# Kernel tuning notes

Measured on AMD Instinct MI355X. Metric: run time of the kernel, lower is better.

## Reference

```python
import jax, jax.numpy as jnp
import numpy as np

B, T, C, H = 4, 2048, 1024, 16
D = C // H


def setup_inputs() -> dict:
    key = jax.random.key(0)
    ks = jax.random.split(key, 5)
    s = 0.02
    return {
        "x": jax.random.normal(ks[0], (B, T, C), dtype=jnp.float32),
        "W_attn": jax.random.normal(ks[1], (C, 3 * C), dtype=jnp.float32) * s,
        "b_attn": jax.random.normal(ks[2], (3 * C,), dtype=jnp.float32) * s,
        "W_proj": jax.random.normal(ks[3], (C, C), dtype=jnp.float32) * s,
        "b_proj": jax.random.normal(ks[4], (C,), dtype=jnp.float32) * s,
    }


def reference(x, W_attn, b_attn, W_proj, b_proj):
    # QKV projection: [B,T,3C]
    qkv = x @ W_attn + b_attn
    q, k, v = jnp.split(qkv, 3, axis=-1)
    # [B,T,C] -> [B,H,T,D]
    def to_heads(t):
        return t.reshape(B, T, H, D).transpose(0, 2, 1, 3)
    q, k, v = to_heads(q), to_heads(k), to_heads(v)
    scale = 1.0 / np.sqrt(D).astype(np.float32)
    # full (non-causal) attention scores [B,H,T,T]
    att = jnp.einsum("bhqd,bhkd->bhqk", q, k) * scale
    att = jax.nn.softmax(att, axis=-1)
    y = jnp.einsum("bhqk,bhkd->bhqd", att, v)
    y = y.transpose(0, 2, 1, 3).reshape(B, T, C)
    return y @ W_proj + b_proj
```

## Files before the change

kernel.cpp:

```cpp
#include <hip/hip_runtime.h>

#define BATCH 4
#define SEQ   2048
#define CDIM  1024
#define NHEAD 16
#define HDIM  64
#define BH    (BATCH * NHEAD)
#define MROWS (BATCH * SEQ)

typedef __attribute__((ext_vector_type(8))) short  short8;
typedef __attribute__((ext_vector_type(4))) float  floatx4;

#define MFMA_BF16(a, b, c) __builtin_amdgcn_mfma_f32_16x16x32_bf16((a), (b), (c), 0, 0, 0)

#define GLOAD16(g, l) __builtin_amdgcn_global_load_lds( \
    (__attribute__((address_space(1))) void*)(g),       \
    (__attribute__((address_space(3))) void*)(l), 16, 0, 0)

__device__ __forceinline__ unsigned short f2bf(float f) {
    union { float f; unsigned u; } v; v.f = f;
    unsigned u = v.u;
    return (unsigned short)((u + 0x7FFFu + ((u >> 16) & 1u)) >> 16);
}

__device__ __forceinline__ float fast_exp2(float x) {
#if __has_builtin(__builtin_amdgcn_exp2f)
    return __builtin_amdgcn_exp2f(x);
#else
    return exp2f(x);
#endif
}

__device__ __forceinline__ unsigned pack_bf16_trunc(float a, float b) {
    union { float f; unsigned u; } ua, ub;
    ua.f = a; ub.f = b;
    return __builtin_amdgcn_perm(ub.u, ua.u, 0x07060302u);
}

__global__ __launch_bounds__(256) void conv_all_kernel(
    const float* __restrict__ x,  unsigned short* __restrict__ xb,
    const float* __restrict__ Wa, unsigned short* __restrict__ Wat,
    const float* __restrict__ Wp, unsigned short* __restrict__ Wpt)
{
    const int bx = blockIdx.x, tid = threadIdx.x;
    if (bx < 8192) {
        int i = (bx * 256 + tid) * 4;
        float4 v = *(const float4*)(x + i);
        ushort4 o;
        o.x = f2bf(v.x); o.y = f2bf(v.y); o.z = f2bf(v.z); o.w = f2bf(v.w);
        *(ushort4*)(xb + i) = o;
        return;
    }
    __shared__ float T[64][68];
    const float* in; unsigned short* out; int N, k0, n0;
    if (bx < 8192 + 768) {
        int t = bx - 8192;
        in = Wa; out = Wat; N = 3 * CDIM;
        n0 = (t % 48) * 64; k0 = (t / 48) * 64;
    } else {
        int t = bx - 8960;
        in = Wp; out = Wpt; N = CDIM;
        n0 = (t & 15) * 64; k0 = (t >> 4) * 64;
    }
    const int K = CDIM;
    const int r = tid >> 4, c4 = (tid & 15) * 4;
    #pragma unroll
    for (int i = 0; i < 4; ++i) {
        int row = r + i * 16;
        float4 v = *(const float4*)(in + (size_t)(k0 + row) * N + n0 + c4);
        T[row][c4 + 0] = v.x; T[row][c4 + 1] = v.y;
        T[row][c4 + 2] = v.z; T[row][c4 + 3] = v.w;
    }
    __syncthreads();
    #pragma unroll
    for (int i = 0; i < 4; ++i) {
        int nrow = r + i * 16;
        ushort4 o;
        o.x = f2bf(T[c4 + 0][nrow]); o.y = f2bf(T[c4 + 1][nrow]);
        o.z = f2bf(T[c4 + 2][nrow]); o.w = f2bf(T[c4 + 3][nrow]);
        *(ushort4*)(out + (size_t)(n0 + nrow) * K + k0 + c4) = o;
    }
}

__global__ __launch_bounds__(512, 2) void qkv_mfma_kernel(
    const unsigned short* __restrict__ A,
    const unsigned short* __restrict__ Bt,
    const float* __restrict__ bias,
    unsigned short* __restrict__ Qo,
    unsigned short* __restrict__ Ko,
    unsigned short* __restrict__ Vo)
{
    __shared__ __align__(16) unsigned short L[2 * 32768];

    const int tid = threadIdx.x;
    const int flat = blockIdx.x;
    const int swz = (flat & 7) * 48 + (flat >> 3);
    const int m0 = (swz / 12) * 256, n0 = (swz % 12) * 256;
    const int w = tid >> 6, lane = tid & 63;
    const int wr = w >> 2, wc = w & 3;
    const int lm = lane & 15, kg = lane >> 4;
    const int sw = lm & 7;

    floatx4 acc[2][4][2][2];
    const floatx4 zf = {0.f, 0.f, 0.f, 0.f};
    #pragma unroll
    for (int a = 0; a < 2; ++a)
        #pragma unroll
        for (int b = 0; b < 4; ++b)
            #pragma unroll
            for (int c = 0; c < 2; ++c)
                #pragma unroll
                for (int d = 0; d < 2; ++d) acc[a][b][c][d] = zf;

    short8 af[4][2], bf[2][2];

#define QSTAGE_A(B_, H_, KT_) do {                                            \
    unsigned short* _l = (unsigned short*)L + (B_) * 32768 + (H_) * 8192;     \
    _Pragma("unroll")                                                         \
    for (int _i = 0; _i < 2; ++_i) {                                          \
        int _s = _i * 512 + tid, _r = _s >> 3, _c = _s & 7;                   \
        GLOAD16(A + (size_t)(m0 + (H_) * 128 + _r) * CDIM + (KT_) * 64        \
                   + ((_c ^ (_r & 7)) * 8), _l + _s * 8);                     \
    } } while (0)

#define QSTAGE_B(B_, H_, KT_) do {                                            \
    unsigned short* _l = (unsigned short*)L + (B_) * 32768 + 16384 + (H_) * 8192; \
    _Pragma("unroll")                                                         \
    for (int _i = 0; _i < 2; ++_i) {                                          \
        int _s = _i * 512 + tid, _r = _s >> 3, _c = _s & 7;                   \
        GLOAD16(Bt + (size_t)(n0 + (H_) * 128 + _r) * CDIM + (KT_) * 64       \
                   + ((_c ^ (_r & 7)) * 8), _l + _s * 8);                     \
    } } while (0)

#define QLOAD_A(B_, H_) do {                                                  \
    const unsigned short* _p = (const unsigned short*)L + (B_) * 32768 + (H_) * 8192; \
    _Pragma("unroll")                                                         \
    for (int _m = 0; _m < 4; ++_m) {                                          \
        int _row = wr * 64 + _m * 16 + lm;                                    \
        _Pragma("unroll")                                                     \
        for (int _k = 0; _k < 2; ++_k)                                        \
            af[_m][_k] = *(const short8*)(_p + _row * 64                      \
                          + (((_k * 4 + kg) ^ sw) * 8));                      \
    } } while (0)

#define QLOAD_B(B_, H_) do {                                                  \
    const unsigned short* _p = (const unsigned short*)L + (B_) * 32768 + 16384 + (H_) * 8192; \
    _Pragma("unroll")                                                         \
    for (int _n = 0; _n < 2; ++_n) {                                          \
        int _row = wc * 32 + _n * 16 + lm;                                    \
        _Pragma("unroll")                                                     \
        for (int _k = 0; _k < 2; ++_k)                                        \
            bf[_n][_k] = *(const short8*)(_p + _row * 64                      \
                          + (((_k * 4 + kg) ^ sw) * 8));                      \
    } } while (0)

#define QMFMA(HH_, HP_) do {                                                  \
    _Pragma("unroll") for (int _k = 0; _k < 2; ++_k)                          \
    _Pragma("unroll") for (int _m = 0; _m < 4; ++_m)                          \
    _Pragma("unroll") for (int _n = 0; _n < 2; ++_n)                          \
        acc[HH_][_m][HP_][_n] =                                               \
            MFMA_BF16(af[_m][_k], bf[_n][_k], acc[HH_][_m][HP_][_n]);         \
    } while (0)

#define QPHASE(HH_, HP_, LA_, LB_, STAGE_, VM_) do {                          \
    if (LA_) QLOAD_A(buf, HH_);                                               \
    if (LB_) QLOAD_B(buf, HP_);                                               \
    STAGE_;                                                                   \
    asm volatile("s_waitcnt vmcnt(" #VM_ ")" ::: "memory");                   \
    __builtin_amdgcn_s_barrier();                                             \
    asm volatile("s_waitcnt lgkmcnt(0)" ::: "memory");                        \
    __builtin_amdgcn_sched_barrier(0);                                        \
    __builtin_amdgcn_s_setprio(1);                                            \
    QMFMA(HH_, HP_);                                                          \
    __builtin_amdgcn_s_setprio(0);                                            \
    __builtin_amdgcn_s_barrier();                                             \
    __builtin_amdgcn_sched_barrier(0);                                        \
    } while (0)

    QSTAGE_A(0, 0, 0); QSTAGE_B(0, 0, 0); QSTAGE_B(0, 1, 0); QSTAGE_A(0, 1, 0);
    asm volatile("s_waitcnt vmcnt(4)" ::: "memory");
    __builtin_amdgcn_s_barrier();

    #pragma unroll 1
    for (int t = 0; t < CDIM / 64 - 1; ++t) {
        const int buf = t & 1, nb = buf ^ 1;
        QPHASE(0, 0, 1, 1, QSTAGE_A(nb, 0, t + 1), 4);
        QPHASE(0, 1, 0, 1, QSTAGE_B(nb, 0, t + 1), 4);
        QPHASE(1, 1, 1, 0, QSTAGE_B(nb, 1, t + 1), 4);
        QPHASE(1, 0, 0, 1, QSTAGE_A(nb, 1, t + 1), 4);
    }
    {
        const int buf = (CDIM / 64 - 1) & 1;
        QPHASE(0, 0, 1, 1, ((void)0), 2);
        QPHASE(0, 1, 0, 1, ((void)0), 0);
        QPHASE(1, 1, 1, 0, ((void)0), 0);
        QPHASE(1, 0, 0, 1, ((void)0), 0);
    }

#undef QPHASE
#undef QMFMA
#undef QLOAD_B
#undef QLOAD_A
#undef QSTAGE_B
#undef QSTAGE_A

    #pragma unroll
    for (int hp = 0; hp < 2; ++hp) {
        #pragma unroll
        for (int nt = 0; nt < 2; ++nt) {
            int col = n0 + hp * 128 + wc * 32 + nt * 16 + lm;
            float bv = bias[col];
            int which = col >> 10;
            int c1 = col & 1023;
            int h = c1 >> 6, d = c1 & 63;
            #pragma unroll
            for (int hh = 0; hh < 2; ++hh) {
                #pragma unroll
                for (int mt = 0; mt < 4; ++mt) {
                    int m = m0 + hh * 128 + wr * 64 + mt * 16 + kg * 4;
                    int b = m >> 11;
                    int tt = m & 2047;
                    int bh = b * NHEAD + h;
                    floatx4 a = acc[hh][mt][hp][nt];
                    if (which == 2) {
                        ushort4 o;
                        o.x = f2bf(a[0] + bv);
                        o.y = f2bf(a[1] + bv);
                        o.z = f2bf(a[2] + bv);
                        o.w = f2bf(a[3] + bv);
                        *(ushort4*)(Vo + ((size_t)bh * 64 + d) * SEQ + tt) = o;
                    } else {
                        unsigned short* dst = (which == 0) ? Qo : Ko;
                        float qs = (which == 0) ? 0.18033688011112042f : 1.0f;
                        #pragma unroll
                        for (int r = 0; r < 4; ++r)
                            dst[((size_t)bh * SEQ + tt + r) * 64 + d] =
                                f2bf((a[r] + bv) * qs);
                    }
                }
            }
        }
    }
}

#define GBUF (128 * 32)

__device__ __forceinline__ void gemm_stage(
    const unsigned short* __restrict__ A, const unsigned short* __restrict__ Bt,
    int K, int m0, int n0, int k0, unsigned short* As, unsigned short* Bs, int tid)
{
    #pragma unroll
    for (int i = 0; i < 2; ++i) {
        int ci = i * 256 + tid;
        GLOAD16(A  + (size_t)(m0 + (ci >> 2)) * K + k0 + (ci & 3) * 8, As + ci * 8);
        GLOAD16(Bt + (size_t)(n0 + (ci >> 2)) * K + k0 + (ci & 3) * 8, Bs + ci * 8);
    }
}

__global__ __launch_bounds__(256) void proj_mfma_kernel(
    const unsigned short* __restrict__ A,
    const unsigned short* __restrict__ Bt,
    const float* __restrict__ bias,
    float* __restrict__ out)
{
    const int K = CDIM;
    __shared__ __align__(16) unsigned short As2[2 * GBUF];
    __shared__ __align__(16) unsigned short Bs2[2 * GBUF];

    const int tid = threadIdx.x;
    const int m0 = blockIdx.y * 128, n0 = blockIdx.x * 128;
    const int w = tid >> 6, lane = tid & 63;
    const int wm = (w >> 1) * 64, wn = (w & 1) * 64;
    const int lm = lane & 15, kg = lane >> 4;

    floatx4 acc[4][4];
    const floatx4 zf = {0.f, 0.f, 0.f, 0.f};
    #pragma unroll
    for (int mt = 0; mt < 4; ++mt)
        #pragma unroll
        for (int nt = 0; nt < 4; ++nt) acc[mt][nt] = zf;

    gemm_stage(A, Bt, K, m0, n0, 0, As2, Bs2, tid);

    #pragma unroll 1
    for (int kt = 0; kt < K / 32; ++kt) {
        __syncthreads();
        if (kt + 1 < K / 32)
            gemm_stage(A, Bt, K, m0, n0, (kt + 1) * 32,
                       As2 + ((kt + 1) & 1) * GBUF, Bs2 + ((kt + 1) & 1) * GBUF, tid);
        const unsigned short* As = As2 + (kt & 1) * GBUF;
        const unsigned short* Bs = Bs2 + (kt & 1) * GBUF;
        short8 af[4], bfr[4];
        #pragma unroll
        for (int t = 0; t < 4; ++t) {
            af[t]  = *(const short8*)(As + (wm + t * 16 + lm) * 32 + kg * 8);
            bfr[t] = *(const short8*)(Bs + (wn + t * 16 + lm) * 32 + kg * 8);
        }
        #pragma unroll
        for (int mt = 0; mt < 4; ++mt)
            #pragma unroll
            for (int nt = 0; nt < 4; ++nt)
                acc[mt][nt] = MFMA_BF16(af[mt], bfr[nt], acc[mt][nt]);
    }

    #pragma unroll
    for (int nt = 0; nt < 4; ++nt) {
        int col = n0 + wn + nt * 16 + lm;
        float bv = bias[col];
        #pragma unroll
        for (int mt = 0; mt < 4; ++mt) {
            int mbase = m0 + wm + mt * 16 + kg * 4;
            #pragma unroll
            for (int r = 0; r < 4; ++r)
                out[(size_t)(mbase + r) * CDIM + col] = acc[mt][nt][r] + bv;
        }
    }
}

#define BUFSH 8192

__device__ __forceinline__ void attn_stage_tile(
    const unsigned short* __restrict__ Kg,
    const unsigned short* __restrict__ Vg,
    size_t base, int kb, unsigned short* buf, int tid)
{
    unsigned short* Kb_ = buf;
    unsigned short* Vb_ = buf + 4096;
    #pragma unroll
    for (int i = 0; i < 2; ++i) {
        int lin = i * 256 + tid;
        int srow = lin >> 3;
        int chunk = lin & 7;
        int s2 = srow & 31;
        int grow = (srow & 32) + ((s2 >> 2) & 3) * 8 + ((s2 >> 4) & 1) * 4 + (s2 & 3);
        int gch = chunk ^ (srow & 7);
        GLOAD16(Kg + base + (size_t)(kb * 64 + grow) * 64 + gch * 8, Kb_ + lin * 8);
        GLOAD16(Vg + base + (size_t)srow * SEQ + kb * 64 + gch * 8, Vb_ + lin * 8);
    }
}

__global__ __launch_bounds__(256) void attn_mfma_kernel(
    const unsigned short* __restrict__ Qg,
    const unsigned short* __restrict__ Kg,
    const unsigned short* __restrict__ Vg,
    unsigned short* __restrict__ Y)
{
    __shared__ __align__(16) unsigned short Smem[2 * BUFSH];

    const int tid = threadIdx.x, w = tid >> 6, lane = tid & 63;
    const int lm = lane & 15, kg = lane >> 4;
    const int qb = blockIdx.x, bh = blockIdx.y;
    const size_t base = (size_t)bh * SEQ * 64;

    short8 qf[2][2];
    #pragma unroll
    for (int nt = 0; nt < 2; ++nt)
        #pragma unroll
        for (int c = 0; c < 2; ++c)
            qf[nt][c] = *(const short8*)(
                Qg + base + (size_t)(qb * 128 + w * 32 + nt * 16 + lm) * 64 + c * 32 + kg * 8);

    const floatx4 zf = {0.f, 0.f, 0.f, 0.f};
    floatx4 O[2][4];
    #pragma unroll
    for (int nt = 0; nt < 2; ++nt)
        #pragma unroll
        for (int nd = 0; nd < 4; ++nd) O[nt][nd] = zf;
    float lsum[2] = {0.f, 0.f};

    attn_stage_tile(Kg, Vg, base, 0, Smem, tid);

    #pragma unroll 1
    for (int kb = 0; kb < SEQ / 64; ++kb) {
        __syncthreads();
        if (kb + 1 < SEQ / 64)
            attn_stage_tile(Kg, Vg, base, kb + 1, Smem + ((kb + 1) & 1) * BUFSH, tid);

        const unsigned short* Ksb = Smem + (kb & 1) * BUFSH;
        const unsigned short* Vsb = Ksb + 4096;
        const int sw = (lm & 7);

        #pragma unroll
        for (int ch = 0; ch < 2; ++ch) {
            uint4 pa[2];
            #pragma unroll
            for (int mt = 0; mt < 2; ++mt) {
                floatx4 st[2];
                #pragma unroll
                for (int nt = 0; nt < 2; ++nt) st[nt] = zf;
                #pragma unroll
                for (int c = 0; c < 2; ++c) {
                    short8 kf = *(const short8*)(
                        Ksb + (ch * 32 + mt * 16 + lm) * 64 + ((c * 4 + kg) ^ sw) * 8);
                    #pragma unroll
                    for (int nt = 0; nt < 2; ++nt)
                        st[nt] = MFMA_BF16(kf, qf[nt][c], st[nt]);
                }
                #pragma unroll
                for (int nt = 0; nt < 2; ++nt) {
                    float e0 = fast_exp2(st[nt][0]);
                    float e1 = fast_exp2(st[nt][1]);
                    float e2 = fast_exp2(st[nt][2]);
                    float e3 = fast_exp2(st[nt][3]);
                    lsum[nt] += (e0 + e1) + (e2 + e3);
                    if (mt == 0) {
                        pa[nt].x = pack_bf16_trunc(e0, e1);
                        pa[nt].y = pack_bf16_trunc(e2, e3);
                    } else {
                        pa[nt].z = pack_bf16_trunc(e0, e1);
                        pa[nt].w = pack_bf16_trunc(e2, e3);
                    }
                }
            }
            #pragma unroll
            for (int nd = 0; nd < 4; ++nd) {
                short8 vb = *(const short8*)(
                    Vsb + (nd * 16 + lm) * 64 + ((ch * 4 + kg) ^ sw) * 8);
                #pragma unroll
                for (int nt = 0; nt < 2; ++nt) {
                    short8 paf;
                    __builtin_memcpy(&paf, &pa[nt], 16);
                    O[nt][nd] = MFMA_BF16(paf, vb, O[nt][nd]);
                }
            }
        }
    }

    #pragma unroll
    for (int nt = 0; nt < 2; ++nt) {
        lsum[nt] += __shfl_xor(lsum[nt], 16);
        lsum[nt] += __shfl_xor(lsum[nt], 32);
    }
    float linv[2][4];
    #pragma unroll
    for (int mq = 0; mq < 2; ++mq)
        #pragma unroll
        for (int r = 0; r < 4; ++r)
            linv[mq][r] = 1.0f / __shfl(lsum[mq], kg * 4 + r);

    const int b = bh >> 4, h = bh & 15;
    #pragma unroll
    for (int mq = 0; mq < 2; ++mq)
        #pragma unroll
        for (int r = 0; r < 4; ++r) {
            int t = qb * 128 + w * 32 + mq * 16 + kg * 4 + r;
            #pragma unroll
            for (int nd = 0; nd < 4; ++nd)
                Y[((size_t)(b * SEQ + t)) * CDIM + h * 64 + nd * 16 + lm] =
                    f2bf(O[mq][nd][r] * linv[mq][r]);
        }
}

extern "C" void kernel_launch(void* const* d_in, const int* in_sizes, int n_in,
                              void* d_out, int out_size, void* d_ws, size_t ws_size,
                              hipStream_t stream) {
    const float* x      = (const float*)d_in[0];
    const float* W_attn = (const float*)d_in[1];
    const float* b_attn = (const float*)d_in[2];
    const float* W_proj = (const float*)d_in[3];
    const float* b_proj = (const float*)d_in[4];
    float* out = (float*)d_out;

    char* ws = (char*)d_ws;
    unsigned short* xb  = (unsigned short*)(ws);
    unsigned short* Wat = (unsigned short*)(ws + (size_t)16777216);
    unsigned short* Wpt = (unsigned short*)(ws + (size_t)23068672);
    unsigned short* Qb  = (unsigned short*)(ws + (size_t)25165824);
    unsigned short* Kb  = (unsigned short*)(ws + (size_t)41943040);
    unsigned short* Vtb = (unsigned short*)(ws + (size_t)58720256);
    unsigned short* Yb  = (unsigned short*)(ws + (size_t)75497472);

    conv_all_kernel<<<dim3(9216), 256, 0, stream>>>(
        x, xb, W_attn, Wat, W_proj, Wpt);

    qkv_mfma_kernel<<<dim3(384), 512, 0, stream>>>(
        xb, Wat, b_attn, Qb, Kb, Vtb);

    attn_mfma_kernel<<<dim3(SEQ / 128, BH), 256, 0, stream>>>(Qb, Kb, Vtb, Yb);

    proj_mfma_kernel<<<dim3(CDIM / 128, MROWS / 128), 256, 0, stream>>>(
        Yb, Wpt, b_proj, out);
}
```

Measured before the change: 269.4 us.

## Share 8-wave 256x128 GEMM pipeline between QKV and output projection kernels

Moves the pipelined 8-wave GEMM body into shared macros with a 256x128 output tile and uses it for both the QKV projection and the output projection. The QKV kernel shrinks from 256x256 tiles to 256x128 and drops its XCD-aware block swizzle, launching a 2D grid of 768 blocks. The projection kernel moves from a simple 256-thread 128x128 double-buffered loop to the 512-thread pipeline with swizzled LDS and global-to-LDS loads. Smaller QKV tiles should give more blocks and better occupancy, at the cost of less data reuse per block and the loss of the swizzle's cache locality.

```diff
diff --git a/kernel.cpp b/kernel.cpp
--- a/kernel.cpp
+++ b/kernel.cpp
@@ -82,6 +82,90 @@
     }
 }
 
+#define LBUF 24576
+
+#define GSTAGE_A(SRC, B_, H_, KT_) do {                                       \
+    unsigned short* _l = (unsigned short*)L + (B_) * LBUF + (H_) * 8192;      \
+    _Pragma("unroll")                                                         \
+    for (int _i = 0; _i < 2; ++_i) {                                          \
+        int _s = _i * 512 + tid, _r = _s >> 3, _c = _s & 7;                   \
+        GLOAD16(SRC + (size_t)(m0 + (H_) * 128 + _r) * CDIM + (KT_) * 64      \
+                   + ((_c ^ (_r & 7)) * 8), _l + _s * 8);                     \
+    } } while (0)
+
+#define GSTAGE_B(SRC, B_, H_, KT_) do {                                       \
+    unsigned short* _l = (unsigned short*)L + (B_) * LBUF + 16384 + (H_) * 4096; \
+    {                                                                         \
+        int _s = tid, _r = _s >> 3, _c = _s & 7;                              \
+        GLOAD16(SRC + (size_t)(n0 + (H_) * 64 + _r) * CDIM + (KT_) * 64       \
+                   + ((_c ^ (_r & 7)) * 8), _l + _s * 8);                     \
+    } } while (0)
+
+#define GLOAD_A(B_, H_) do {                                                  \
+    const unsigned short* _p = (const unsigned short*)L + (B_) * LBUF + (H_) * 8192; \
+    _Pragma("unroll")                                                         \
+    for (int _m = 0; _m < 4; ++_m) {                                          \
+        int _row = wr * 64 + _m * 16 + lm;                                    \
+        _Pragma("unroll")                                                     \
+        for (int _k = 0; _k < 2; ++_k)                                        \
+            af[_m][_k] = *(const short8*)(_p + _row * 64                      \
+                          + (((_k * 4 + kg) ^ sw) * 8));                      \
+    } } while (0)
+
+#define GLOAD_B(B_, H_) do {                                                  \
+    const unsigned short* _p = (const unsigned short*)L + (B_) * LBUF + 16384 + (H_) * 4096; \
+    {                                                                         \
+        int _row = wc * 16 + lm;                                              \
+        _Pragma("unroll")                                                     \
+        for (int _k = 0; _k < 2; ++_k)                                        \
+            bf[_k] = *(const short8*)(_p + _row * 64                          \
+                          + (((_k * 4 + kg) ^ sw) * 8));                      \
+    } } while (0)
+
+#define GMFMA(HH_, HP_) do {                                                  \
+    _Pragma("unroll") for (int _k = 0; _k < 2; ++_k)                          \
+    _Pragma("unroll") for (int _m = 0; _m < 4; ++_m)                          \
+        acc[HH_][_m][HP_] =                                                   \
+            MFMA_BF16(af[_m][_k], bf[_k], acc[HH_][_m][HP_]);                 \
+    } while (0)
+
+#define GPHASE(HH_, HP_, LA_, LB_, STAGE_, VM_) do {                          \
+    if (LA_) GLOAD_A(buf, HH_);                                               \
+    if (LB_) GLOAD_B(buf, HP_);                                               \
+    STAGE_;                                                                   \
+    asm volatile("s_waitcnt vmcnt(" #VM_ ")" ::: "memory");                   \
+    __builtin_amdgcn_s_barrier();                                             \
+    asm volatile("s_waitcnt lgkmcnt(0)" ::: "memory");                        \
+    __builtin_amdgcn_sched_barrier(0);                                        \
+    __builtin_amdgcn_s_setprio(1);                                            \
+    GMFMA(HH_, HP_);                                                          \
+    __builtin_amdgcn_s_setprio(0);                                            \
+    __builtin_amdgcn_s_barrier();                                             \
+    __builtin_amdgcn_sched_barrier(0);                                        \
+    } while (0)
+
+#define GEMM_BODY(ASRC, BSRC)                                                 \
+          \
+    GSTAGE_A(ASRC, 0, 0, 0); GSTAGE_B(BSRC, 0, 0, 0);                         \
+    GSTAGE_B(BSRC, 0, 1, 0); GSTAGE_A(ASRC, 0, 1, 0);                         \
+    asm volatile("s_waitcnt vmcnt(2)" ::: "memory");                          \
+    __builtin_amdgcn_s_barrier();                                             \
+    _Pragma("unroll 1")                                                       \
+    for (int t = 0; t < CDIM / 64 - 1; ++t) {                                 \
+        const int buf = t & 1, nb = buf ^ 1;                                  \
+        GPHASE(0, 0, 1, 1, GSTAGE_A(ASRC, nb, 0, t + 1), 3);                  \
+        GPHASE(0, 1, 0, 1, GSTAGE_B(BSRC, nb, 0, t + 1), 3);                  \
+        GPHASE(1, 1, 1, 0, GSTAGE_B(BSRC, nb, 1, t + 1), 2);                  \
+        GPHASE(1, 0, 0, 1, GSTAGE_A(ASRC, nb, 1, t + 1), 2);                  \
+    }                                                                         \
+    {              \
+        const int buf = (CDIM / 64 - 1) & 1;                                  \
+        GPHASE(0, 0, 1, 1, ((void)0), 1);                                     \
+        GPHASE(0, 1, 0, 1, ((void)0), 0);                                     \
+        GPHASE(1, 1, 1, 0, ((void)0), 0);                                     \
+        GPHASE(1, 0, 0, 1, ((void)0), 0);                                     \
+    }
+
 __global__ __launch_bounds__(512, 2) void qkv_mfma_kernel(
     const unsigned short* __restrict__ A,
     const unsigned short* __restrict__ Bt,
@@ -90,229 +174,106 @@
     unsigned short* __restrict__ Ko,
     unsigned short* __restrict__ Vo)
 {
-    __shared__ __align__(16) unsigned short L[2 * 32768];
+    __shared__ __align__(16) unsigned short L[2 * LBUF];
 
     const int tid = threadIdx.x;
-    const int flat = blockIdx.x;
-    const int swz = (flat & 7) * 48 + (flat >> 3);
-    const int m0 = (swz / 12) * 256, n0 = (swz % 12) * 256;
+    const int m0 = blockIdx.y * 256, n0 = blockIdx.x * 128;
     const int w = tid >> 6, lane = tid & 63;
     const int wr = w >> 2, wc = w & 3;
     const int lm = lane & 15, kg = lane >> 4;
     const int sw = lm & 7;
 
-    floatx4 acc[2][4][2][2];
+    floatx4 acc[2][4][2];
     const floatx4 zf = {0.f, 0.f, 0.f, 0.f};
     #pragma unroll
     for (int a = 0; a < 2; ++a)
         #pragma unroll
         for (int b = 0; b < 4; ++b)
             #pragma unroll
-            for (int c = 0; c < 2; ++c)
-                #pragma unroll
-                for (int d = 0; d < 2; ++d) acc[a][b][c][d] = zf;
-
-    short8 af[4][2], bf[2][2];
-
-#define QSTAGE_A(B_, H_, KT_) do {                                            \
-    unsigned short* _l = (unsigned short*)L + (B_) * 32768 + (H_) * 8192;     \
-    _Pragma("unroll")                                                         \
-    for (int _i = 0; _i < 2; ++_i) {                                          \
-        int _s = _i * 512 + tid, _r = _s >> 3, _c = _s & 7;                   \
-        GLOAD16(A + (size_t)(m0 + (H_) * 128 + _r) * CDIM + (KT_) * 64        \
-                   + ((_c ^ (_r & 7)) * 8), _l + _s * 8);                     \
-    } } while (0)
-
-#define QSTAGE_B(B_, H_, KT_) do {                                            \
-    unsigned short* _l = (unsigned short*)L + (B_) * 32768 + 16384 + (H_) * 8192; \
-    _Pragma("unroll")                                                         \
-    for (int _i = 0; _i < 2; ++_i) {                                          \
-        int _s = _i * 512 + tid, _r = _s >> 3, _c = _s & 7;                   \
-        GLOAD16(Bt + (size_t)(n0 + (H_) * 128 + _r) * CDIM + (KT_) * 64       \
-                   + ((_c ^ (_r & 7)) * 8), _l + _s * 8);                     \
-    } } while (0)
-
-#define QLOAD_A(B_, H_) do {                                                  \
-    const unsigned short* _p = (const unsigned short*)L + (B_) * 32768 + (H_) * 8192; \
-    _Pragma("unroll")                                                         \
-    for (int _m = 0; _m < 4; ++_m) {                                          \
-        int _row = wr * 64 + _m * 16 + lm;                                    \
-        _Pragma("unroll")                                                     \
-        for (int _k = 0; _k < 2; ++_k)                                        \
-            af[_m][_k] = *(const short8*)(_p + _row * 64                      \
-                          + (((_k * 4 + kg) ^ sw) * 8));                      \
-    } } while (0)
-
-#define QLOAD_B(B_, H_) do {                                                  \
-    const unsigned short* _p = (const unsigned short*)L + (B_) * 32768 + 16384 + (H_) * 8192; \
-    _Pragma("unroll")                                                         \
-    for (int _n = 0; _n < 2; ++_n) {                                          \
-        int _row = wc * 32 + _n * 16 + lm;                                    \
-        _Pragma("unroll")                                                     \
-        for (int _k = 0; _k < 2; ++_k)                                        \
-            bf[_n][_k] = *(const short8*)(_p + _row * 64                      \
-                          + (((_k * 4 + kg) ^ sw) * 8));                      \
-    } } while (0)
-
-#define QMFMA(HH_, HP_) do {                                                  \
-    _Pragma("unroll") for (int _k = 0; _k < 2; ++_k)                          \
-    _Pragma("unroll") for (int _m = 0; _m < 4; ++_m)                          \
-    _Pragma("unroll") for (int _n = 0; _n < 2; ++_n)                          \
-        acc[HH_][_m][HP_][_n] =                                               \
-            MFMA_BF16(af[_m][_k], bf[_n][_k], acc[HH_][_m][HP_][_n]);         \
-    } while (0)
-
-#define QPHASE(HH_, HP_, LA_, LB_, STAGE_, VM_) do {                          \
-    if (LA_) QLOAD_A(buf, HH_);                                               \
-    if (LB_) QLOAD_B(buf, HP_);                                               \
-    STAGE_;                                                                   \
-    asm volatile("s_waitcnt vmcnt(" #VM_ ")" ::: "memory");                   \
-    __builtin_amdgcn_s_barrier();                                             \
-    asm volatile("s_waitcnt lgkmcnt(0)" ::: "memory");                        \
-    __builtin_amdgcn_sched_barrier(0);                                        \
-    __builtin_amdgcn_s_setprio(1);                                            \
-    QMFMA(HH_, HP_);                                                          \
-    __builtin_amdgcn_s_setprio(0);                                            \
-    __builtin_amdgcn_s_barrier();                                             \
-    __builtin_amdgcn_sched_barrier(0);                                        \
-    } while (0)
-
-    QSTAGE_A(0, 0, 0); QSTAGE_B(0, 0, 0); QSTAGE_B(0, 1, 0); QSTAGE_A(0, 1, 0);
-    asm volatile("s_waitcnt vmcnt(4)" ::: "memory");
-    __builtin_amdgcn_s_barrier();
-
-    #pragma unroll 1
-    for (int t = 0; t < CDIM / 64 - 1; ++t) {
-        const int buf = t & 1, nb = buf ^ 1;
-        QPHASE(0, 0, 1, 1, QSTAGE_A(nb, 0, t + 1), 4);
-        QPHASE(0, 1, 0, 1, QSTAGE_B(nb, 0, t + 1), 4);
-        QPHASE(1, 1, 1, 0, QSTAGE_B(nb, 1, t + 1), 4);
-        QPHASE(1, 0, 0, 1, QSTAGE_A(nb, 1, t + 1), 4);
-    }
-    {
-        const int buf = (CDIM / 64 - 1) & 1;
-        QPHASE(0, 0, 1, 1, ((void)0), 2);
-        QPHASE(0, 1, 0, 1, ((void)0), 0);
-        QPHASE(1, 1, 1, 0, ((void)0), 0);
-        QPHASE(1, 0, 0, 1, ((void)0), 0);
-    }
-
-#undef QPHASE
-#undef QMFMA
-#undef QLOAD_B
-#undef QLOAD_A
-#undef QSTAGE_B
-#undef QSTAGE_A
+            for (int c = 0; c < 2; ++c) acc[a][b][c] = zf;
+
+    short8 af[4][2], bf[2];
+
+    GEMM_BODY(A, Bt)
 
     #pragma unroll
     for (int hp = 0; hp < 2; ++hp) {
-        #pragma unroll
-        for (int nt = 0; nt < 2; ++nt) {
-            int col = n0 + hp * 128 + wc * 32 + nt * 16 + lm;
-            float bv = bias[col];
-            int which = col >> 10;
-            int c1 = col & 1023;
-            int h = c1 >> 6, d = c1 & 63;
-            #pragma unroll
-            for (int hh = 0; hh < 2; ++hh) {
-                #pragma unroll
-                for (int mt = 0; mt < 4; ++mt) {
-                    int m = m0 + hh * 128 + wr * 64 + mt * 16 + kg * 4;
-                    int b = m >> 11;
-                    int tt = m & 2047;
-                    int bh = b * NHEAD + h;
-                    floatx4 a = acc[hh][mt][hp][nt];
-                    if (which == 2) {
-                        ushort4 o;
-                        o.x = f2bf(a[0] + bv);
-                        o.y = f2bf(a[1] + bv);
-                        o.z = f2bf(a[2] + bv);
-                        o.w = f2bf(a[3] + bv);
-                        *(ushort4*)(Vo + ((size_t)bh * 64 + d) * SEQ + tt) = o;
-                    } else {
-                        unsigned short* dst = (which == 0) ? Qo : Ko;
-                        float qs = (which == 0) ? 0.18033688011112042f : 1.0f;
-                        #pragma unroll
-                        for (int r = 0; r < 4; ++r)
-                            dst[((size_t)bh * SEQ + tt + r) * 64 + d] =
-                                f2bf((a[r] + bv) * qs);
-                    }
+        int col = n0 + hp * 64 + wc * 16 + lm;
+        float bv = bias[col];
+        int which = col >> 10;
+        int c1 = col & 1023;
+        int h = c1 >> 6, d = c1 & 63;
+        #pragma unroll
+        for (int hh = 0; hh < 2; ++hh) {
+            #pragma unroll
+            for (int mt = 0; mt < 4; ++mt) {
+                int m = m0 + hh * 128 + wr * 64 + mt * 16 + kg * 4;
+                int b = m >> 11;
+                int tt = m & 2047;
+                int bh = b * NHEAD + h;
+                floatx4 a = acc[hh][mt][hp];
+                if (which == 2) {
+                    ushort4 o;
+                    o.x = f2bf(a[0] + bv);
+                    o.y = f2bf(a[1] + bv);
+                    o.z = f2bf(a[2] + bv);
+                    o.w = f2bf(a[3] + bv);
+                    *(ushort4*)(Vo + ((size_t)bh * 64 + d) * SEQ + tt) = o;
+                } else {
+                    unsigned short* dst = (which == 0) ? Qo : Ko;
+                    float qs = (which == 0) ? 0.18033688011112042f : 1.0f;
+                    #pragma unroll
+                    for (int r = 0; r < 4; ++r)
+                        dst[((size_t)bh * SEQ + tt + r) * 64 + d] =
+                            f2bf((a[r] + bv) * qs);
                 }
             }
         }
     }
 }
 
-#define GBUF (128 * 32)
-
-__device__ __forceinline__ void gemm_stage(
-    const unsigned short* __restrict__ A, const unsigned short* __restrict__ Bt,
-    int K, int m0, int n0, int k0, unsigned short* As, unsigned short* Bs, int tid)
-{
-    #pragma unroll
-    for (int i = 0; i < 2; ++i) {
-        int ci = i * 256 + tid;
-        GLOAD16(A  + (size_t)(m0 + (ci >> 2)) * K + k0 + (ci & 3) * 8, As + ci * 8);
-        GLOAD16(Bt + (size_t)(n0 + (ci >> 2)) * K + k0 + (ci & 3) * 8, Bs + ci * 8);
-    }
-}
-
-__global__ __launch_bounds__(256) void proj_mfma_kernel(
+__global__ __launch_bounds__(512, 2) void proj_mfma_kernel(
     const unsigned short* __restrict__ A,
     const unsigned short* __restrict__ Bt,
     const float* __restrict__ bias,
     float* __restrict__ out)
 {
-    const int K = CDIM;
-    __shared__ __align__(16) unsigned short As2[2 * GBUF];
-    __shared__ __align__(16) unsigned short Bs2[2 * GBUF];
+    __shared__ __align__(16) unsigned short L[2 * LBUF];
 
     const int tid = threadIdx.x;
-    const int m0 = blockIdx.y * 128, n0 = blockIdx.x * 128;
+    const int m0 = blockIdx.y * 256, n0 = blockIdx.x * 128;
     const int w = tid >> 6, lane = tid & 63;
-    const int wm = (w >> 1) * 64, wn = (w & 1) * 64;
+    const int wr = w >> 2, wc = w & 3;
     const int lm = lane & 15, kg = lane >> 4;
-
-    floatx4 acc[4][4];
+    const int sw = lm & 7;
+
+    floatx4 acc[2][4][2];
     const floatx4 zf = {0.f, 0.f, 0.f, 0.f};
     #pragma unroll
-    for (int mt = 0; mt < 4; ++mt)
-        #pragma unroll
-        for (int nt = 0; nt < 4; ++nt) acc[mt][nt] = zf;
-
-    gemm_stage(A, Bt, K, m0, n0, 0, As2, Bs2, tid);
-
-    #pragma unroll 1
-    for (int kt = 0; kt < K / 32; ++kt) {
-        __syncthreads();
-        if (kt + 1 < K / 32)
-            gemm_stage(A, Bt, K, m0, n0, (kt + 1) * 32,
-                       As2 + ((kt + 1) & 1) * GBUF, Bs2 + ((kt + 1) & 1) * GBUF, tid);
-        const unsigned short* As = As2 + (kt & 1) * GBUF;
-        const unsigned short* Bs = Bs2 + (kt & 1) * GBUF;
-        short8 af[4], bfr[4];
-        #pragma unroll
-        for (int t = 0; t < 4; ++t) {
-            af[t]  = *(const short8*)(As + (wm + t * 16 + lm) * 32 + kg * 8);
-            bfr[t] = *(const short8*)(Bs + (wn + t * 16 + lm) * 32 + kg * 8);
-        }
-        #pragma unroll
-        for (int mt = 0; mt < 4; ++mt)
-            #pragma unroll
-            for (int nt = 0; nt < 4; ++nt)
-                acc[mt][nt] = MFMA_BF16(af[mt], bfr[nt], acc[mt][nt]);
-    }
-
-    #pragma unroll
-    for (int nt = 0; nt < 4; ++nt) {
-        int col = n0 + wn + nt * 16 + lm;
+    for (int a = 0; a < 2; ++a)
+        #pragma unroll
+        for (int b = 0; b < 4; ++b)
+            #pragma unroll
+            for (int c = 0; c < 2; ++c) acc[a][b][c] = zf;
+
+    short8 af[4][2], bf[2];
+
+    GEMM_BODY(A, Bt)
+
+    #pragma unroll
+    for (int hp = 0; hp < 2; ++hp) {
+        int col = n0 + hp * 64 + wc * 16 + lm;
         float bv = bias[col];
         #pragma unroll
-        for (int mt = 0; mt < 4; ++mt) {
-            int mbase = m0 + wm + mt * 16 + kg * 4;
-            #pragma unroll
-            for (int r = 0; r < 4; ++r)
-                out[(size_t)(mbase + r) * CDIM + col] = acc[mt][nt][r] + bv;
+        for (int hh = 0; hh < 2; ++hh) {
+            #pragma unroll
+            for (int mt = 0; mt < 4; ++mt) {
+                int row = m0 + hh * 128 + wr * 64 + mt * 16 + kg * 4;
+                floatx4 a = acc[hh][mt][hp];
+                #pragma unroll
+                for (int r = 0; r < 4; ++r)
+                    out[(size_t)(row + r) * CDIM + col] = a[r] + bv;
+            }
         }
     }
 }
@@ -473,11 +434,11 @@
     conv_all_kernel<<<dim3(9216), 256, 0, stream>>>(
         x, xb, W_attn, Wat, W_proj, Wpt);
 
-    qkv_mfma_kernel<<<dim3(384), 512, 0, stream>>>(
+    qkv_mfma_kernel<<<dim3(3 * CDIM / 128, MROWS / 256), 512, 0, stream>>>(
         xb, Wat, b_attn, Qb, Kb, Vtb);
 
     attn_mfma_kernel<<<dim3(SEQ / 128, BH), 256, 0, stream>>>(Qb, Kb, Vtb, Yb);
 
-    proj_mfma_kernel<<<dim3(CDIM / 128, MROWS / 128), 256, 0, stream>>>(
+    proj_mfma_kernel<<<dim3(CDIM / 128, MROWS / 256), 512, 0, stream>>>(
         Yb, Wpt, b_proj, out);
 }
```

New measurement: 275.5 us. +2.3%, slower.
